# Optimization experiments

Hardware: AMD Instinct MI355X
Metric: run time of the kernel (lower is better)

The kernel has to match this reference:

```python
import jax, jax.numpy as jnp
import numpy as np

B = 65536
D_MODEL = 2048
N_EXPERTS = 64
TOP_K = 8
AUX_COEF = 0.01


def setup_inputs() -> dict:
    key = jax.random.key(0)
    kx, kw = jax.random.split(key)
    x = jax.random.normal(kx, (B, D_MODEL), dtype=jnp.float32)
    # nn.Linear(d_model, n_experts, bias=False); stored here as (d_model, n_experts)
    W = jax.random.normal(kw, (D_MODEL, N_EXPERTS), dtype=jnp.float32) / np.sqrt(D_MODEL).astype(np.float32)
    expert_bias = jnp.zeros((N_EXPERTS,), dtype=jnp.float32)
    return {"x": x, "W": W, "expert_bias": expert_bias}


def reference(x, W, expert_bias):
    # router logits: (B, n_experts)
    logits = x @ W
    # topk on bias-shifted logits (aux-loss-free balancing bias)
    biased = logits + expert_bias
    _, indices = jax.lax.top_k(biased, TOP_K)              # (B, top_k) int32
    # softmax over the UNbiased logits of the selected experts
    selected = jnp.take_along_axis(logits, indices, axis=-1)  # (B, top_k)
    gates_topk = jax.nn.softmax(selected, axis=-1)
    # scatter gate weights into sparse (B, n_experts) tensor
    rows = jnp.arange(logits.shape[0])[:, None]
    gates = jnp.zeros_like(logits).at[rows, indices].set(gates_topk)
    # aux load-balance loss (training mode): fraction routed * mean prob
    f_i = (gates > 0).astype(logits.dtype).mean(axis=0)       # (n_experts,)
    P_i = jax.nn.softmax(logits, axis=-1).mean(axis=0)        # (n_experts,)
    aux_loss = AUX_COEF * N_EXPERTS * jnp.sum(f_i * P_i)
    return gates, indices, aux_loss
```

## Files before the change

kernel.cpp:

```cpp
#include <hip/hip_runtime.h>
#include <cstdint>
#include <cstddef>

typedef __attribute__((ext_vector_type(8))) short short8;
typedef __attribute__((ext_vector_type(4))) float f32x4;

#define B_ROWS 65536
#define DMODEL 2048
#define NEXP 64
#define TOPK 8
#define THREADS 512
#define ROWS_PER_BLK 128
#define NBLK (B_ROWS / ROWS_PER_BLK)
#define NKS (DMODEL / 32)
#define NITER (NKS / 2)
#define SLAB 67
#define GOFF ((size_t)B_ROWS * NEXP)
#define AUX_OFF (GOFF + (size_t)B_ROWS * TOPK)
#define WS_FRAG_OFF 131072
#define WS2_OFF 229376

#define GLOAD16(g, l)                                                      \
  __builtin_amdgcn_global_load_lds(                                       \
      (const __attribute__((address_space(1))) void*)(g),                 \
      (__attribute__((address_space(3))) void*)(l), 16, 0, 0)

__device__ __forceinline__ unsigned short bf16_rne(float v, float* back) {
  unsigned u = __float_as_uint(v);
  unsigned r = (u + 0x7FFFu + ((u >> 16) & 1u)) >> 16;
  *back = __uint_as_float(r << 16);
  return (unsigned short)r;
}

__global__ __launch_bounds__(256) void router_prep(
    const float* __restrict__ W, unsigned short* __restrict__ frag)
{
  const int ks = blockIdx.x;
  const int nt = threadIdx.x >> 6;
  const int lane = threadIdx.x & 63;
  const int krow = ks * 32 + (lane >> 4) * 8;
  const int col = nt * 16 + (lane & 15);
  short8 hv, mv, lv;
#pragma unroll
  for (int j = 0; j < 8; ++j) {
    float v = W[(size_t)(krow + j) * NEXP + col];
    float fh, fm, fl;
    unsigned short h = bf16_rne(v, &fh);
    float r = v - fh;
    unsigned short m = bf16_rne(r, &fm);
    float r2 = r - fm;
    unsigned short l = bf16_rne(r2, &fl);
    hv[j] = (short)h; mv[j] = (short)m; lv[j] = (short)l;
  }
  size_t base = (size_t)(ks * 4 + nt) * 1536 + lane * 8;
  *(short8*)(frag + base)        = hv;
  *(short8*)(frag + base + 512)  = mv;
  *(short8*)(frag + base + 1024) = lv;
}

__device__ __forceinline__ void cvt3(float4 a, float4 b,
                                     short8* H, short8* M, short8* L) {
  float f[8] = {a.x, a.y, a.z, a.w, b.x, b.y, b.z, b.w};
#pragma unroll
  for (int j = 0; j < 8; ++j) {
    float fh, fm, fl;
    unsigned short h = bf16_rne(f[j], &fh);
    float r = f[j] - fh;
    unsigned short m = bf16_rne(r, &fm);
    float r2 = r - fm;
    unsigned short l = bf16_rne(r2, &fl);
    (*H)[j] = (short)h; (*M)[j] = (short)m; (*L)[j] = (short)l;
  }
}

#define MFMA __builtin_amdgcn_mfma_f32_16x16x32_bf16

__global__ __launch_bounds__(THREADS, 4) void router_main(
    const float* __restrict__ x, const float* __restrict__ bias,
    const unsigned short* __restrict__ frag, float* __restrict__ out,
    float* __restrict__ ws)
{
  __shared__ __align__(16) float lds[2 * 6144];

  const int tid = threadIdx.x;
  const int lane = tid & 63;
  const int w = tid >> 6;
  const size_t row0 = (size_t)blockIdx.x * ROWS_PER_BLK;

  f32x4 acc[4];
#pragma unroll
  for (int nt = 0; nt < 4; ++nt) acc[nt] = (f32x4){0.f, 0.f, 0.f, 0.f};

  const float* xp = x + (row0 + (size_t)w * 16 + (lane & 15)) * DMODEL
                  + (lane >> 4) * 8;

#define STAGE_BPAIR(G, BUF)                                                \
  do {                                                                     \
    _Pragma("unroll") for (int j = 0; j < 3; ++j)                          \
      GLOAD16(frag + (size_t)(G) * 12288 + (w * 3 + j) * 512 + lane * 8,   \
              lds + (BUF) * 6144 + (w * 3 + j) * 256);                     \
  } while (0)

#define LOAD_BL(BB, NT, BH, BM, BL)                                        \
  do {                                                                     \
    const float* p_ = (BB) + (NT) * 768 + lane * 4;                        \
    BH = *(const short8*)(p_);                                             \
    BM = *(const short8*)(p_ + 256);                                       \
    BL = *(const short8*)(p_ + 512);                                       \
  } while (0)

#define MFMA12(NT, BH, BM, BL)                                             \
  do {                                                                     \
    acc[NT] = MFMA(Ah, BH, acc[NT], 0, 0, 0);                              \
    acc[NT] = MFMA(Ah, BM, acc[NT], 0, 0, 0);                              \
    acc[NT] = MFMA(Am, BH, acc[NT], 0, 0, 0);                              \
    acc[NT] = MFMA(Am, BM, acc[NT], 0, 0, 0);                              \
    acc[NT] = MFMA(Ah, BL, acc[NT], 0, 0, 0);                              \
    acc[NT] = MFMA(Al, BH, acc[NT], 0, 0, 0);                              \
  } while (0)

#define COMPUTE_KS(G, KK, C0, C1)                                          \
  do {                                                                     \
    const float* bb = lds + ((G) & 1) * 6144 + (KK) * 3072;                \
    short8 Ah, Am, Al;                                                     \
    cvt3(C0, C1, &Ah, &Am, &Al);                                           \
    short8 BhA, BmA, BlA, BhB, BmB, BlB;                                   \
    LOAD_BL(bb, 0, BhA, BmA, BlA);                                         \
    LOAD_BL(bb, 1, BhB, BmB, BlB);                                         \
    MFMA12(0, BhA, BmA, BlA);                                              \
    LOAD_BL(bb, 2, BhA, BmA, BlA);                                         \
    MFMA12(1, BhB, BmB, BlB);                                              \
    LOAD_BL(bb, 3, BhB, BmB, BlB);                                         \
    MFMA12(2, BhA, BmA, BlA);                                              \
    MFMA12(3, BhB, BmB, BlB);                                              \
  } while (0)

#define XLOAD(G, V0, V1, V2, V3)                                           \
  do {                                                                     \
    V0 = *(const float4*)(xp + (G) * 64);                                  \
    V1 = *(const float4*)(xp + (G) * 64 + 4);                              \
    V2 = *(const float4*)(xp + (G) * 64 + 32);                             \
    V3 = *(const float4*)(xp + (G) * 64 + 36);                             \
  } while (0)

#define ITER_HEAD(G)                                                       \
  do {                                                                     \
    asm volatile("s_waitcnt vmcnt(4)" ::: "memory");                       \
    __builtin_amdgcn_sched_barrier(0);                                     \
    __builtin_amdgcn_s_barrier();                                          \
  } while (0)

  float4 a0, a1, a2, a3, b0, b1, b2, b3;
  STAGE_BPAIR(0, 0);
  XLOAD(0, a0, a1, a2, a3);

  for (int g2 = 0; g2 < 16; ++g2) {
    {
      const int g = 2 * g2;
      ITER_HEAD(g);
      STAGE_BPAIR(g + 1, (g + 1) & 1);
      XLOAD(g + 1, b0, b1, b2, b3);
      COMPUTE_KS(g, 0, a0, a1);
      COMPUTE_KS(g, 1, a2, a3);
    }
    {
      const int g = 2 * g2 + 1;
      ITER_HEAD(g);
      if (g + 1 < NITER) {
        STAGE_BPAIR(g + 1, (g + 1) & 1);
        XLOAD(g + 1, a0, a1, a2, a3);
      }
      COMPUTE_KS(g, 0, b0, b1);
      COMPUTE_KS(g, 1, b2, b3);
    }
  }

  __syncthreads();
  float* slab = lds;
#pragma unroll
  for (int nt = 0; nt < 4; ++nt)
#pragma unroll
    for (int reg = 0; reg < 4; ++reg) {
      int row = w * 16 + (lane >> 4) * 4 + reg;
      int col = nt * 16 + (lane & 15);
      slab[row * SLAB + col] = acc[nt][reg];
    }
  __syncthreads();

  float* redF = lds + ROWS_PER_BLK * SLAB;
  float* redP = redF + 128;

  if (w < 2) {
    const int row = w * 64 + lane;
    float a[NEXP];
#pragma unroll
    for (int n = 0; n < NEXP; ++n) a[n] = slab[row * SLAB + n];

    unsigned long long sel = 0ull;
    int idx[TOPK];
    float selu[TOPK];
#pragma unroll
    for (int k = 0; k < TOPK; ++k) {
      float best = -INFINITY, bestu = 0.f;
      int bi = 0;
#pragma unroll
      for (int n = 0; n < NEXP; ++n) {
        float vb = a[n] + bias[n];
        bool taken = (sel >> n) & 1ull;
        vb = taken ? -INFINITY : vb;
        if (vb > best) { best = vb; bestu = a[n]; bi = n; }
      }
      sel |= 1ull << bi;
      idx[k] = bi;
      selu[k] = bestu;
    }

    float mx = selu[0];
#pragma unroll
    for (int k = 1; k < TOPK; ++k) mx = fmaxf(mx, selu[k]);
    float g[TOPK]; float gs = 0.f;
#pragma unroll
    for (int k = 0; k < TOPK; ++k) { g[k] = __expf(selu[k] - mx); gs += g[k]; }
    float ginv = 1.f / gs;

    float* grow = out + (row0 + row) * NEXP;
#pragma unroll
    for (int n4 = 0; n4 < 16; ++n4) {
      float gv[4];
#pragma unroll
      for (int j = 0; j < 4; ++j) {
        int n = n4 * 4 + j;
        float v = 0.f;
#pragma unroll
        for (int k = 0; k < TOPK; ++k) v = (idx[k] == n) ? g[k] * ginv : v;
        gv[j] = v;
      }
      *(float4*)(grow + n4 * 4) = make_float4(gv[0], gv[1], gv[2], gv[3]);
    }

    float* irow = out + GOFF + (row0 + row) * TOPK;
    *(float4*)(irow + 0) = make_float4((float)idx[0], (float)idx[1], (float)idx[2], (float)idx[3]);
    *(float4*)(irow + 4) = make_float4((float)idx[4], (float)idx[5], (float)idx[6], (float)idx[7]);

    float m2 = -INFINITY;
#pragma unroll
    for (int n = 0; n < NEXP; ++n) m2 = fmaxf(m2, a[n]);
    float s2 = 0.f;
#pragma unroll
    for (int n = 0; n < NEXP; ++n) s2 += __expf(a[n] - m2);
    float pinv = 1.f / s2;

    float myP = 0.f, myF = 0.f;
#pragma unroll
    for (int n = 0; n < NEXP; ++n) {
      float v = __expf(a[n] - m2) * pinv;
      v += __shfl_xor(v, 1);
      v += __shfl_xor(v, 2);
      v += __shfl_xor(v, 4);
      v += __shfl_xor(v, 8);
      v += __shfl_xor(v, 16);
      v += __shfl_xor(v, 32);
      unsigned long long b = __ballot((sel >> n) & 1ull);
      if (lane == n) { myP = v; myF = (float)__popcll(b); }
    }
    redF[w * 64 + lane] = myF;
    redP[w * 64 + lane] = myP;
  }

  __syncthreads();
  if (tid < NEXP) {
    float F = redF[tid] + redF[64 + tid];
    float P = redP[tid] + redP[64 + tid];
    ws[(size_t)blockIdx.x * (2 * NEXP) + tid] = F;
    ws[(size_t)blockIdx.x * (2 * NEXP) + NEXP + tid] = P;
  }
}

__global__ __launch_bounds__(256) void router_aux1(
    const float* __restrict__ ws, float* __restrict__ ws2)
{
  __shared__ float sf[4][NEXP];
  __shared__ float sp[4][NEXP];
  int t = threadIdx.x;
  int n = t & 63, part = t >> 6;
  int b0 = blockIdx.x * 32;
  float f = 0.f, p = 0.f;
#pragma unroll 4
  for (int b = b0 + part; b < b0 + 32; b += 4) {
    f += ws[(size_t)b * (2 * NEXP) + n];
    p += ws[(size_t)b * (2 * NEXP) + NEXP + n];
  }
  sf[part][n] = f;
  sp[part][n] = p;
  __syncthreads();
  if (t < NEXP) {
    ws2[blockIdx.x * 128 + t]      = sf[0][t] + sf[1][t] + sf[2][t] + sf[3][t];
    ws2[blockIdx.x * 128 + 64 + t] = sp[0][t] + sp[1][t] + sp[2][t] + sp[3][t];
  }
}

__global__ __launch_bounds__(64) void router_aux2(
    const float* __restrict__ ws2, float* __restrict__ out)
{
  int t = threadIdx.x;
  float F = 0.f, P = 0.f;
#pragma unroll
  for (int g = 0; g < 16; ++g) {
    F += ws2[g * 128 + t];
    P += ws2[g * 128 + 64 + t];
  }
  float v = F * P;
  v += __shfl_xor(v, 1);
  v += __shfl_xor(v, 2);
  v += __shfl_xor(v, 4);
  v += __shfl_xor(v, 8);
  v += __shfl_xor(v, 16);
  v += __shfl_xor(v, 32);
  if (t == 0)
    out[AUX_OFF] = 0.01f * 64.f * v / (4294967296.0f );
}

extern "C" void kernel_launch(void* const* d_in, const int* in_sizes, int n_in,
                              void* d_out, int out_size, void* d_ws, size_t ws_size,
                              hipStream_t stream) {
  const float* x = (const float*)d_in[0];
  const float* W = (const float*)d_in[1];
  const float* bias = (const float*)d_in[2];
  float* out = (float*)d_out;
  float* ws = (float*)d_ws;
  unsigned short* frag = (unsigned short*)(ws + WS_FRAG_OFF);
  float* ws2 = ws + WS2_OFF;
  router_prep<<<NKS, 256, 0, stream>>>(W, frag);
  router_main<<<NBLK, THREADS, 0, stream>>>(x, bias, frag, out, ws);
  router_aux1<<<16, 256, 0, stream>>>(ws, ws2);
  router_aux2<<<1, 64, 0, stream>>>(ws2, out);
}
```

Before: 206.4 us.

## Deepen x prefetch to two iterations with triple-buffered registers

Rotates three sets of x register buffers so global loads for iteration g+2 are issued while iteration g computes, instead of prefetching only one step ahead. The intent is more bytes in flight per wave to hide HBM latency on this bandwidth-bound GEMV-like router. The launch-bounds occupancy hint drops from 4 to 3 blocks per CU so the extra live registers fit. The risk is that fewer resident waves cancel out the deeper per-wave prefetch.

```diff
diff --git a/kernel.cpp b/kernel.cpp
--- a/kernel.cpp
+++ b/kernel.cpp
@@ -75,7 +75,7 @@
 
 #define MFMA __builtin_amdgcn_mfma_f32_16x16x32_bf16
 
-__global__ __launch_bounds__(THREADS, 4) void router_main(
+__global__ __launch_bounds__(THREADS, 3) void router_main(
     const float* __restrict__ x, const float* __restrict__ bias,
     const unsigned short* __restrict__ frag, float* __restrict__ out,
     float* __restrict__ ws)
@@ -143,36 +143,43 @@
     V3 = *(const float4*)(xp + (G) * 64 + 36);                             \
   } while (0)
 
-#define ITER_HEAD(G)                                                       \
-  do {                                                                     \
-    asm volatile("s_waitcnt vmcnt(4)" ::: "memory");                       \
+#define ITER_HEAD_N(VM)                                                    \
+  do {                                                                     \
+    asm volatile("s_waitcnt vmcnt(" #VM ")" ::: "memory");                 \
     __builtin_amdgcn_sched_barrier(0);                                     \
     __builtin_amdgcn_s_barrier();                                          \
   } while (0)
 
-  float4 a0, a1, a2, a3, b0, b1, b2, b3;
+#define ITER3(G, U0, U1, U2, U3, L0, L1, L2, L3)                           \
+  do {                                                                     \
+    ITER_HEAD_N(4);                                                        \
+    STAGE_BPAIR((G) + 1, ((G) + 1) & 1);                                   \
+    XLOAD((G) + 2, L0, L1, L2, L3);                                        \
+    COMPUTE_KS(G, 0, U0, U1);                                              \
+    COMPUTE_KS(G, 1, U2, U3);                                              \
+  } while (0)
+
+  float4 a0, a1, a2, a3, b0, b1, b2, b3, c0, c1, c2, c3;
   STAGE_BPAIR(0, 0);
   XLOAD(0, a0, a1, a2, a3);
-
-  for (int g2 = 0; g2 < 16; ++g2) {
-    {
-      const int g = 2 * g2;
-      ITER_HEAD(g);
-      STAGE_BPAIR(g + 1, (g + 1) & 1);
-      XLOAD(g + 1, b0, b1, b2, b3);
-      COMPUTE_KS(g, 0, a0, a1);
-      COMPUTE_KS(g, 1, a2, a3);
-    }
-    {
-      const int g = 2 * g2 + 1;
-      ITER_HEAD(g);
-      if (g + 1 < NITER) {
-        STAGE_BPAIR(g + 1, (g + 1) & 1);
-        XLOAD(g + 1, a0, a1, a2, a3);
-      }
-      COMPUTE_KS(g, 0, b0, b1);
-      COMPUTE_KS(g, 1, b2, b3);
-    }
+  XLOAD(1, b0, b1, b2, b3);
+
+  for (int g3 = 0; g3 < 10; ++g3) {
+    const int g = 3 * g3;
+    ITER3(g,     a0, a1, a2, a3, c0, c1, c2, c3);
+    ITER3(g + 1, b0, b1, b2, b3, a0, a1, a2, a3);
+    ITER3(g + 2, c0, c1, c2, c3, b0, b1, b2, b3);
+  }
+  {
+    ITER_HEAD_N(4);
+    STAGE_BPAIR(31, 1);
+    COMPUTE_KS(30, 0, a0, a1);
+    COMPUTE_KS(30, 1, a2, a3);
+  }
+  {
+    ITER_HEAD_N(0);
+    COMPUTE_KS(31, 0, b0, b1);
+    COMPUTE_KS(31, 1, b2, b3);
   }
 
   __syncthreads();
```

Measured after the change: 262.2 us. 1.27x slower.
